# Optimization experiments

Measured on AMD Instinct MI355X. Metric: run time of the kernel, lower is better.

## Reference

```python
import jax, jax.numpy as jnp
import numpy as np

GRID_N = 3   # number of grid intervals (pykan 'grid')
K = 3        # spline order (pykan 'k')
IN_F = 512
OUT_F = 512
BATCH = 8
SEQ = 2048


def _extended_grid(d, dtype):
    # base grid: num+1 points over [-1, 1]; extend by K steps of h on each side (pykan extend_grid)
    pts = jnp.linspace(-1.0, 1.0, GRID_N + 1).astype(dtype)
    h = jnp.asarray(2.0 / GRID_N, dtype)
    left = pts[0] + h * jnp.arange(-K, 0, dtype=dtype)
    right = pts[-1] + h * jnp.arange(1, K + 1, dtype=dtype)
    ext = jnp.concatenate([left, pts, right])           # (GRID_N + 1 + 2K,)
    return jnp.broadcast_to(ext, (d, ext.shape[0]))     # per-input-feature grid (shared values)


def _bspline_basis(x, grid):
    # Cox-de Boor recursion, vectorized over tokens and input features.
    # x: (N, D), grid: (D, M) -> returns (N, D, M-1-K) = (N, D, GRID_N+K)
    x = x[:, :, None]                     # (N, D, 1)
    g = grid[None, :, :]                  # (1, D, M)
    B = ((x >= g[..., :-1]) & (x < g[..., 1:])).astype(x.dtype)
    for p in range(1, K + 1):
        left = (x - g[..., :-(p + 1)]) / (g[..., p:-1] - g[..., :-(p + 1)])
        right = (g[..., p + 1:] - x) / (g[..., p + 1:] - g[..., 1:-p])
        B = left * B[..., :-1] + right * B[..., 1:]
    return B


def setup_inputs() -> dict:
    key = jax.random.key(0)
    k1, k2, k3 = jax.random.split(key, 3)
    x = jax.random.normal(k1, (BATCH, SEQ, IN_F), dtype=jnp.float32)
    coef = jax.random.normal(k2, (OUT_F, IN_F, GRID_N + K), dtype=jnp.float32) * 0.1
    scale_base = (1.0 / np.sqrt(IN_F)) + (jax.random.uniform(k3, (OUT_F, IN_F), dtype=jnp.float32) * 2.0 - 1.0) * 0.1
    scale_sp = jnp.ones((OUT_F, IN_F), dtype=jnp.float32)
    bias = jnp.zeros((OUT_F,), dtype=jnp.float32)
    return {"x": x, "coef": coef, "scale_base": scale_base, "scale_sp": scale_sp, "bias": bias}


def reference(x, coef, scale_base, scale_sp, bias):
    B_, S, D = x.shape
    xf = x.reshape(-1, D)                               # (N, D) tokens
    grid = _extended_grid(D, xf.dtype)
    basis = _bspline_basis(xf, grid)                    # (N, D, GRID_N+K)
    base = jax.nn.silu(xf)                              # base activation per input feature
    # per-edge: scale_base*silu(x_i) + scale_sp*spline(x_i); sum over input features, add bias
    spline_w = scale_sp[..., None] * coef               # (O, D, GRID_N+K)
    y = (jnp.einsum('ni,oi->no', base, scale_base)
         + jnp.einsum('nib,oib->no', basis, spline_w)
         + bias[None, :])
    return y.reshape(B_, S, -1)
```

## Files before the change

kernel.cpp:

```cpp
#include <hip/hip_runtime.h>


typedef short        bf16x8 __attribute__((ext_vector_type(8)));
typedef float        f32x4  __attribute__((ext_vector_type(4)));
typedef unsigned int u32x4  __attribute__((ext_vector_type(4)));

#define NROWS 16384
#define DIN   512
#define DOUT  512
#define BM    64
#define BN    256
#define NKT   64
#define WT_TILE_BYTES 32768

__device__ __forceinline__ unsigned short f2bf(float f) {
    unsigned int u = __float_as_uint(f);
    u += 0x7fffu + ((u >> 16) & 1u);
    return (unsigned short)(u >> 16);
}

__device__ __forceinline__ void kan_act_store(float xv, char* p16) {
    float S  = __builtin_fmaf(xv, 1.5f, 4.5f);
    float jf = floorf(S);
    float t  = S - jf;
    int   j  = (int)jf;
    float t2 = t * t;
    float t3 = t2 * t;
    float omt  = 1.0f - t;
    float omt2 = omt * omt;
    float n0 = omt2 * omt * (1.0f / 6.0f);
    float n1 = __builtin_fmaf(t3, 0.5f, -t2) + (2.0f / 3.0f);
    float u  = (t + t2) - t3;
    float n2 = __builtin_fmaf(u, 0.5f, 1.0f / 6.0f);
    float n3 = t3 * (1.0f / 6.0f);
    float e  = __expf(-xv);
    float si = xv * __builtin_amdgcn_rcpf(1.0f + e);

    unsigned w01, w23, wsil;
    asm("v_cvt_pk_bf16_f32 %0, %1, %2" : "=v"(w01)  : "v"(n0), "v"(n1));
    asm("v_cvt_pk_bf16_f32 %0, %1, %2" : "=v"(w23)  : "v"(n2), "v"(n3));
    asm("v_cvt_pk_bf16_f32 %0, %1, %2" : "=v"(wsil) : "v"(si), "v"(0.0f));

    u32x4 init = {wsil, 0u, 0u, 0u};
    *(u32x4*)p16 = init;

    unsigned short v0 = (unsigned short)w01, v1 = (unsigned short)(w01 >> 16);
    unsigned short v2 = (unsigned short)w23, v3 = (unsigned short)(w23 >> 16);
    int b0 = j - 3;
    int s0 = ((unsigned)(b0    ) <= 5u) ? (b0 + 1) : 7;
    int s1 = ((unsigned)(b0 + 1) <= 5u) ? (b0 + 2) : 7;
    int s2 = ((unsigned)(b0 + 2) <= 5u) ? (b0 + 3) : 7;
    int s3 = ((unsigned)(b0 + 3) <= 5u) ? (b0 + 4) : 7;
    *(unsigned short*)(p16 + 2 * s0) = v0;
    *(unsigned short*)(p16 + 2 * s1) = v1;
    *(unsigned short*)(p16 + 2 * s2) = v2;
    *(unsigned short*)(p16 + 2 * s3) = v3;
}

__global__ __launch_bounds__(256) void kan_prep(
    const float* __restrict__ coef, const float* __restrict__ scale_base,
    const float* __restrict__ scale_sp, unsigned short* __restrict__ wt)
{
    int t = blockIdx.x * 256 + threadIdx.x;
    int o = t >> 9;
    int i = t & 511;
    float sb = scale_base[t];
    float sp = scale_sp[t];
    const float* cp = coef + (size_t)t * 6;
    bf16x8 w;
    w[0] = (short)f2bf(sb);
#pragma unroll
    for (int b = 0; b < 6; ++b) w[1 + b] = (short)f2bf(sp * cp[b]);
    w[7] = 0;
    int nt = o >> 8;
    int ol = o & 255;
    int kt = i >> 3;
    int colbyte = (i & 7) << 4;
    unsigned off = (unsigned)((nt * NKT + kt) * WT_TILE_BYTES
                              + ol * 128 + (colbyte ^ ((ol & 7) << 4)));
    *(bf16x8*)((char*)wt + off) = w;
}

__device__ __forceinline__ void gload_lds16(const void* g, void* l) {
    __builtin_amdgcn_global_load_lds(
        (const __attribute__((address_space(1))) void*)g,
        (__attribute__((address_space(3))) void*)l, 16, 0, 0);
}

__global__ __launch_bounds__(256, 2) void kan_gemm(
    const float* __restrict__ x, const unsigned short* __restrict__ wt,
    const float* __restrict__ bias, float* __restrict__ y)
{
    __shared__ char As[2][BM * 128];
    __shared__ char Ws[2][BN * 128];

    const int tid  = threadIdx.x;
    const int lane = tid & 63;
    const int wid  = tid >> 6;

    int bid = blockIdx.x;
    int wg  = (bid & 7) * 64 + (bid >> 3);
    int mt  = wg & 255;
    int nt  = wg >> 8;

    const int row0 = mt * BM;
    const int col0 = nt * BN;

    const int ar = tid >> 2;
    const int ap = tid & 3;
    const float* xp = x + (size_t)(row0 + ar) * DIN + ap * 2;
    const int as_sw = (ar & 7) << 4;
    const int c0 = (ap * 2) << 4;

    const char* wsrc = (const char*)wt + (size_t)nt * NKT * WT_TILE_BYTES;

    f32x4 acc[4][4];
#pragma unroll
    for (int m2 = 0; m2 < 4; ++m2)
#pragma unroll
        for (int n2 = 0; n2 < 4; ++n2) {
            f32x4 z = {0.f, 0.f, 0.f, 0.f};
            acc[m2][n2] = z;
        }

    const int fr = lane & 15;
    const int fg = lane >> 4;

    float2 xa = *(const float2*)(xp);
    {
        const char* s = wsrc + wid * 1024 + lane * 16;
        char* d = &Ws[0][wid * 1024];
#pragma unroll
        for (int q = 0; q < 8; ++q)
            gload_lds16(s + q * 4096, d + q * 4096);
        char* rowp = &As[0][ar * 128];
        kan_act_store(xa.x, rowp + (c0 ^ as_sw));
        kan_act_store(xa.y, rowp + ((c0 + 16) ^ as_sw));
    }
    float2 xb = *(const float2*)(xp + 8);
    asm volatile("s_waitcnt lgkmcnt(0)" ::: "memory");
    __builtin_amdgcn_s_barrier();

    int cur = 0;
    for (int kt = 0; kt < NKT; ++kt) {
        const int nxt = cur ^ 1;
        const bool has_next = (kt + 1 < NKT);

        if (has_next) {
            const char* s = wsrc + (kt + 1) * WT_TILE_BYTES + wid * 1024 + lane * 16;
            char* d = &Ws[nxt][wid * 1024];
#pragma unroll
            for (int q = 0; q < 8; ++q)
                gload_lds16(s + q * 4096, d + q * 4096);
            asm volatile("s_waitcnt vmcnt(9)" ::: "memory");
        } else {
            asm volatile("s_waitcnt vmcnt(0)" ::: "memory");
        }

        bf16x8 af[2][4], bf[2][4];
#pragma unroll
        for (int ks = 0; ks < 2; ++ks) {
            const int cb = ks * 64 + fg * 16;
#pragma unroll
            for (int m2 = 0; m2 < 4; ++m2) {
                int rr = m2 * 16 + fr;
                af[ks][m2] = *(const bf16x8*)(&As[cur][0] + rr * 128 + (cb ^ ((rr & 7) << 4)));
            }
#pragma unroll
            for (int n2 = 0; n2 < 4; ++n2) {
                int wr = wid * 64 + n2 * 16 + fr;
                bf[ks][n2] = *(const bf16x8*)(&Ws[cur][0] + wr * 128 + (cb ^ ((wr & 7) << 4)));
            }
        }

        if (has_next) {
            char* rowp = &As[nxt][ar * 128];
            kan_act_store(xb.x, rowp + (c0 ^ as_sw));
            kan_act_store(xb.y, rowp + ((c0 + 16) ^ as_sw));
            if (kt + 2 < NKT)
                xb = *(const float2*)(xp + (kt + 2) * 8);
        }

#pragma unroll
        for (int ks = 0; ks < 2; ++ks)
#pragma unroll
            for (int m2 = 0; m2 < 4; ++m2)
#pragma unroll
                for (int n2 = 0; n2 < 4; ++n2)
                    acc[m2][n2] = __builtin_amdgcn_mfma_f32_16x16x32_bf16(
                        af[ks][m2], bf[ks][n2], acc[m2][n2], 0, 0, 0);

        asm volatile("s_waitcnt lgkmcnt(0)" ::: "memory");
        __builtin_amdgcn_s_barrier();
        cur = nxt;
    }

    const int orow0 = row0 + fg * 4;
    const int ocol0 = col0 + wid * 64 + fr;
#pragma unroll
    for (int n2 = 0; n2 < 4; ++n2) {
        float bv = bias[ocol0 + n2 * 16];
#pragma unroll
        for (int m2 = 0; m2 < 4; ++m2) {
#pragma unroll
            for (int r = 0; r < 4; ++r) {
                y[(size_t)(orow0 + m2 * 16 + r) * DOUT + (ocol0 + n2 * 16)]
                    = acc[m2][n2][r] + bv;
            }
        }
    }
}

extern "C" void kernel_launch(void* const* d_in, const int* in_sizes, int n_in,
                              void* d_out, int out_size, void* d_ws, size_t ws_size,
                              hipStream_t stream)
{
    const float* x          = (const float*)d_in[0];
    const float* coef       = (const float*)d_in[1];
    const float* scale_base = (const float*)d_in[2];
    const float* scale_sp   = (const float*)d_in[3];
    const float* bias       = (const float*)d_in[4];
    unsigned short* wt = (unsigned short*)d_ws;
    float* y = (float*)d_out;

    kan_prep<<<1024, 256, 0, stream>>>(coef, scale_base, scale_sp, wt);
    kan_gemm<<<512, 256, 0, stream>>>(x, wt, bias, y);
}
```

Measured before the change: 96.14 us.

## Load weight fragments straight to registers and double the row tile

The weight tile no longer goes through LDS. Each wave loads its bf16 B fragments directly from global memory into registers from a plain row-major weight buffer, with one k-step of register prefetch via ping-pong buffers. The row tile grows to 128 with 512-thread blocks, arranged as a 2x4 wave grid, and the grid shrinks to 256 blocks. This removes the LDS write/read traffic for the weights and frees LDS space. In exchange, waves in the two row halves fetch the same weights redundantly from cache, and the direct loads may expose more memory latency.

```diff
diff --git a/kernel.cpp b/kernel.cpp
--- a/kernel.cpp
+++ b/kernel.cpp
@@ -8,10 +8,9 @@
 #define NROWS 16384
 #define DIN   512
 #define DOUT  512
-#define BM    64
+#define BM    128
 #define BN    256
 #define NKT   64
-#define WT_TILE_BYTES 32768
 
 __device__ __forceinline__ unsigned short f2bf(float f) {
     unsigned int u = __float_as_uint(f);
@@ -62,8 +61,6 @@
     const float* __restrict__ scale_sp, unsigned short* __restrict__ wt)
 {
     int t = blockIdx.x * 256 + threadIdx.x;
-    int o = t >> 9;
-    int i = t & 511;
     float sb = scale_base[t];
     float sp = scale_sp[t];
     const float* cp = coef + (size_t)t * 6;
@@ -72,36 +69,25 @@
 #pragma unroll
     for (int b = 0; b < 6; ++b) w[1 + b] = (short)f2bf(sp * cp[b]);
     w[7] = 0;
-    int nt = o >> 8;
-    int ol = o & 255;
-    int kt = i >> 3;
-    int colbyte = (i & 7) << 4;
-    unsigned off = (unsigned)((nt * NKT + kt) * WT_TILE_BYTES
-                              + ol * 128 + (colbyte ^ ((ol & 7) << 4)));
-    *(bf16x8*)((char*)wt + off) = w;
-}
-
-__device__ __forceinline__ void gload_lds16(const void* g, void* l) {
-    __builtin_amdgcn_global_load_lds(
-        (const __attribute__((address_space(1))) void*)g,
-        (__attribute__((address_space(3))) void*)l, 16, 0, 0);
-}
-
-__global__ __launch_bounds__(256, 2) void kan_gemm(
+    *(bf16x8*)((char*)wt + (size_t)t * 16) = w;
+}
+
+__global__ __launch_bounds__(512, 2) void kan_gemm(
     const float* __restrict__ x, const unsigned short* __restrict__ wt,
     const float* __restrict__ bias, float* __restrict__ y)
 {
     __shared__ char As[2][BM * 128];
-    __shared__ char Ws[2][BN * 128];
 
     const int tid  = threadIdx.x;
     const int lane = tid & 63;
     const int wid  = tid >> 6;
+    const int wm   = wid >> 2;
+    const int wn   = wid & 3;
 
     int bid = blockIdx.x;
-    int wg  = (bid & 7) * 64 + (bid >> 3);
-    int mt  = wg & 255;
-    int nt  = wg >> 8;
+    int wg  = (bid & 7) * 32 + (bid >> 3);
+    int mt  = wg & 127;
+    int nt  = wg >> 7;
 
     const int row0 = mt * BM;
     const int col0 = nt * BN;
@@ -112,7 +98,26 @@
     const int as_sw = (ar & 7) << 4;
     const int c0 = (ap * 2) << 4;
 
-    const char* wsrc = (const char*)wt + (size_t)nt * NKT * WT_TILE_BYTES;
+    const int fr = lane & 15;
+    const int fg = lane >> 4;
+
+    const char* wb = (const char*)wt;
+    size_t bbase[4];
+#pragma unroll
+    for (int n2 = 0; n2 < 4; ++n2) {
+        int o = col0 + wn * 64 + n2 * 16 + fr;
+        bbase[n2] = ((size_t)o * 512 + fg) * 16;
+    }
+
+#define LOADB(B, ktv)                                                         \
+    {                                                                         \
+        _Pragma("unroll")                                                     \
+        for (int q = 0; q < 8; ++q) {                                         \
+            int n2_ = q & 3, ks_ = q >> 2;                                    \
+            B[q] = *(const bf16x8*)(wb + bbase[n2_]                           \
+                                    + (size_t)((ktv) * 8 + ks_ * 4) * 16);    \
+        }                                                                     \
+    }
 
     f32x4 acc[4][4];
 #pragma unroll
@@ -123,80 +128,60 @@
             acc[m2][n2] = z;
         }
 
-    const int fr = lane & 15;
-    const int fg = lane >> 4;
-
-    float2 xa = *(const float2*)(xp);
+    bf16x8 Ba[8], Bb[8];
+
     {
-        const char* s = wsrc + wid * 1024 + lane * 16;
-        char* d = &Ws[0][wid * 1024];
-#pragma unroll
-        for (int q = 0; q < 8; ++q)
-            gload_lds16(s + q * 4096, d + q * 4096);
+        float2 xa = *(const float2*)(xp);
         char* rowp = &As[0][ar * 128];
         kan_act_store(xa.x, rowp + (c0 ^ as_sw));
         kan_act_store(xa.y, rowp + ((c0 + 16) ^ as_sw));
     }
+    LOADB(Ba, 0);
     float2 xb = *(const float2*)(xp + 8);
     asm volatile("s_waitcnt lgkmcnt(0)" ::: "memory");
     __builtin_amdgcn_s_barrier();
 
-    int cur = 0;
-    for (int kt = 0; kt < NKT; ++kt) {
-        const int nxt = cur ^ 1;
-        const bool has_next = (kt + 1 < NKT);
-
-        if (has_next) {
-            const char* s = wsrc + (kt + 1) * WT_TILE_BYTES + wid * 1024 + lane * 16;
-            char* d = &Ws[nxt][wid * 1024];
-#pragma unroll
-            for (int q = 0; q < 8; ++q)
-                gload_lds16(s + q * 4096, d + q * 4096);
-            asm volatile("s_waitcnt vmcnt(9)" ::: "memory");
-        } else {
-            asm volatile("s_waitcnt vmcnt(0)" ::: "memory");
-        }
-
-        bf16x8 af[2][4], bf[2][4];
-#pragma unroll
-        for (int ks = 0; ks < 2; ++ks) {
-            const int cb = ks * 64 + fg * 16;
-#pragma unroll
-            for (int m2 = 0; m2 < 4; ++m2) {
-                int rr = m2 * 16 + fr;
-                af[ks][m2] = *(const bf16x8*)(&As[cur][0] + rr * 128 + (cb ^ ((rr & 7) << 4)));
-            }
-#pragma unroll
-            for (int n2 = 0; n2 < 4; ++n2) {
-                int wr = wid * 64 + n2 * 16 + fr;
-                bf[ks][n2] = *(const bf16x8*)(&Ws[cur][0] + wr * 128 + (cb ^ ((wr & 7) << 4)));
-            }
-        }
-
-        if (has_next) {
-            char* rowp = &As[nxt][ar * 128];
-            kan_act_store(xb.x, rowp + (c0 ^ as_sw));
-            kan_act_store(xb.y, rowp + ((c0 + 16) ^ as_sw));
-            if (kt + 2 < NKT)
-                xb = *(const float2*)(xp + (kt + 2) * 8);
-        }
-
-#pragma unroll
-        for (int ks = 0; ks < 2; ++ks)
-#pragma unroll
-            for (int m2 = 0; m2 < 4; ++m2)
-#pragma unroll
-                for (int n2 = 0; n2 < 4; ++n2)
-                    acc[m2][n2] = __builtin_amdgcn_mfma_f32_16x16x32_bf16(
-                        af[ks][m2], bf[ks][n2], acc[m2][n2], 0, 0, 0);
-
-        asm volatile("s_waitcnt lgkmcnt(0)" ::: "memory");
-        __builtin_amdgcn_s_barrier();
-        cur = nxt;
-    }
-
-    const int orow0 = row0 + fg * 4;
-    const int ocol0 = col0 + wid * 64 + fr;
+#define STEP(ktv, Bcur, Bnext)                                                \
+    {                                                                         \
+        const int cur_ = (ktv) & 1, nxt_ = cur_ ^ 1;                          \
+        if ((ktv) + 1 < NKT) {                                                \
+            LOADB(Bnext, (ktv) + 1);                                          \
+            char* rowp_ = &As[nxt_][ar * 128];                                \
+            kan_act_store(xb.x, rowp_ + (c0 ^ as_sw));                        \
+            kan_act_store(xb.y, rowp_ + ((c0 + 16) ^ as_sw));                 \
+            if ((ktv) + 2 < NKT)                                              \
+                xb = *(const float2*)(xp + ((ktv) + 2) * 8);                  \
+        }                                                                     \
+        bf16x8 af_[2][4];                                                     \
+        _Pragma("unroll")                                                     \
+        for (int ks_ = 0; ks_ < 2; ++ks_) {                                   \
+            _Pragma("unroll")                                                 \
+            for (int m2_ = 0; m2_ < 4; ++m2_) {                               \
+                int rr_ = wm * 64 + m2_ * 16 + fr;                            \
+                af_[ks_][m2_] = *(const bf16x8*)(&As[cur_][0] + rr_ * 128     \
+                    + ((ks_ * 64 + fg * 16) ^ ((rr_ & 7) << 4)));             \
+            }                                                                 \
+        }                                                                     \
+        _Pragma("unroll")                                                     \
+        for (int ks_ = 0; ks_ < 2; ++ks_)                                     \
+            _Pragma("unroll")                                                 \
+            for (int m2_ = 0; m2_ < 4; ++m2_)                                 \
+                _Pragma("unroll")                                             \
+                for (int n2_ = 0; n2_ < 4; ++n2_)                             \
+                    acc[m2_][n2_] = __builtin_amdgcn_mfma_f32_16x16x32_bf16(  \
+                        af_[ks_][m2_], Bcur[ks_ * 4 + n2_], acc[m2_][n2_],    \
+                        0, 0, 0);                                             \
+        asm volatile("s_waitcnt lgkmcnt(0)" ::: "memory");                    \
+        __builtin_amdgcn_s_barrier();                                         \
+    }
+
+    for (int kt = 0; kt < NKT; kt += 2) {
+        STEP(kt, Ba, Bb);
+        STEP(kt + 1, Bb, Ba);
+    }
+
+    const int orow0 = row0 + wm * 64 + fg * 4;
+    const int ocol0 = col0 + wn * 64 + fr;
 #pragma unroll
     for (int n2 = 0; n2 < 4; ++n2) {
         float bv = bias[ocol0 + n2 * 16];
@@ -209,6 +194,8 @@
             }
         }
     }
+#undef STEP
+#undef LOADB
 }
 
 extern "C" void kernel_launch(void* const* d_in, const int* in_sizes, int n_in,
@@ -224,5 +211,5 @@
     float* y = (float*)d_out;
 
     kan_prep<<<1024, 256, 0, stream>>>(coef, scale_base, scale_sp, wt);
-    kan_gemm<<<512, 256, 0, stream>>>(x, wt, bias, y);
-}
+    kan_gemm<<<256, 512, 0, stream>>>(x, wt, bias, y);
+}
```

Measured after the change: 149.6 us. +55.6%, slower.
